# Optimization experiments

Hardware: AMD Instinct MI355X
Metric: run time of the kernel (lower is better)

The kernel has to match this reference:

```python
import jax, jax.numpy as jnp
import numpy as np

N, E, G = 100000, 1600000, 128
IN, HID, HEADS, EDIM, OUT = 16, 32, 4, 8, 4
HC = HEADS * HID


def _p(k, shape):
    return jax.random.normal(k, shape, jnp.float32) * 0.1


def setup_inputs():
    key = jax.random.key(0)
    ks = list(jax.random.split(key, 24))
    nxt = iter(ks)
    d = dict(
        x=jax.random.normal(next(nxt), (N, IN), jnp.float32),
        edge_index=jax.random.randint(next(nxt), (2, E), 0, N),
        edge_attr=jax.random.normal(next(nxt), (E, EDIM), jnp.float32),
        batch=jnp.sort(jax.random.randint(next(nxt), (N,), 0, G)),
    )
    # conv1: in=IN -> heads*hid
    d['wl1'] = _p(next(nxt), (IN, HC));  d['bl1'] = jnp.zeros((HC,), jnp.float32)
    d['wr1'] = _p(next(nxt), (IN, HC));  d['br1'] = jnp.zeros((HC,), jnp.float32)
    d['we1'] = _p(next(nxt), (EDIM, HC)); d['att1'] = _p(next(nxt), (HEADS, HID)); d['bc1'] = jnp.zeros((HC,), jnp.float32)
    # conv2: in=HC -> heads*hid
    d['wl2'] = _p(next(nxt), (HC, HC));  d['bl2'] = jnp.zeros((HC,), jnp.float32)
    d['wr2'] = _p(next(nxt), (HC, HC));  d['br2'] = jnp.zeros((HC,), jnp.float32)
    d['we2'] = _p(next(nxt), (EDIM, HC)); d['att2'] = _p(next(nxt), (HEADS, HID)); d['bc2'] = jnp.zeros((HC,), jnp.float32)
    # conv3: in=HC -> 1*hid (heads=1)
    d['wl3'] = _p(next(nxt), (HC, HID)); d['bl3'] = jnp.zeros((HID,), jnp.float32)
    d['wr3'] = _p(next(nxt), (HC, HID)); d['br3'] = jnp.zeros((HID,), jnp.float32)
    d['we3'] = _p(next(nxt), (EDIM, HID)); d['att3'] = _p(next(nxt), (1, HID)); d['bc3'] = jnp.zeros((HID,), jnp.float32)
    d['w_fc1'] = _p(next(nxt), (HID, 2 * HID)); d['b_fc1'] = jnp.zeros((2 * HID,), jnp.float32)
    d['w_fc2'] = _p(next(nxt), (2 * HID, OUT)); d['b_fc2'] = jnp.zeros((OUT,), jnp.float32)
    return d


def _gatv2(x, src, dst, eattr, wl, bl, wr, br, we, att, bias, n):
    # PyG GATv2Conv: e_ij = a^T . leaky_relu(Wl x_j + Wr x_i + We e_ij)
    H, C = att.shape
    xl = (x @ wl + bl).reshape(-1, H, C)  # source transform [N,H,C]
    xr = (x @ wr + br).reshape(-1, H, C)  # target transform [N,H,C]
    ea = (eattr @ we).reshape(-1, H, C)   # edge transform   [E,H,C]
    e = jax.nn.leaky_relu(xl[src] + xr[dst] + ea, 0.2)  # [E,H,C]
    logit = jnp.einsum('ehc,hc->eh', e, att)            # [E,H]
    m = jax.ops.segment_max(logit, dst, num_segments=n)
    p = jnp.exp(logit - m[dst])
    s = jax.ops.segment_sum(p, dst, num_segments=n)
    alpha = p / (s[dst] + 1e-16)                        # segment softmax per dst
    out = jax.ops.segment_sum(xl[src] * alpha[:, :, None], dst, num_segments=n)
    return out.reshape(n, H * C) + bias


def reference(x, edge_index, edge_attr, batch,
              wl1, bl1, wr1, br1, we1, att1, bc1,
              wl2, bl2, wr2, br2, we2, att2, bc2,
              wl3, bl3, wr3, br3, we3, att3, bc3,
              w_fc1, b_fc1, w_fc2, b_fc2):
    n = x.shape[0]
    src, dst = edge_index[0], edge_index[1]
    # add_self_loops=True with fill_value='mean' (mean of incoming edge_attr per node)
    ones_e = jnp.ones((src.shape[0],), x.dtype)
    cnt = jax.ops.segment_sum(ones_e, dst, num_segments=n)
    loop_attr = jax.ops.segment_sum(edge_attr, dst, num_segments=n) / jnp.maximum(cnt, 1.0)[:, None]
    ar = jnp.arange(n)
    src_a = jnp.concatenate([src, ar])
    dst_a = jnp.concatenate([dst, ar])
    ea = jnp.concatenate([edge_attr, loop_attr], axis=0)

    h = jax.nn.elu(_gatv2(x, src_a, dst_a, ea, wl1, bl1, wr1, br1, we1, att1, bc1, n))
    h = jax.nn.elu(_gatv2(h, src_a, dst_a, ea, wl2, bl2, wr2, br2, we2, att2, bc2, n))
    h = jax.nn.elu(_gatv2(h, src_a, dst_a, ea, wl3, bl3, wr3, br3, we3, att3, bc3, n))

    # global mean pool over graphs
    gs = jax.ops.segment_sum(h, batch, num_segments=G)
    gc = jax.ops.segment_sum(jnp.ones((n,), h.dtype), batch, num_segments=G)
    g = gs / jnp.maximum(gc, 1.0)[:, None]

    g = jax.nn.elu(g @ w_fc1 + b_fc1)
    return g @ w_fc2 + b_fc2
```

## Files before the change

### kernel.cpp

```cpp
#include <hip/hip_runtime.h>
#include <cstdint>
#include <type_traits>

constexpr int GNUM = 128;

typedef _Float16 h2 __attribute__((ext_vector_type(2)));
typedef _Float16 h4 __attribute__((ext_vector_type(4)));
typedef _Float16 h8 __attribute__((ext_vector_type(8)));
typedef float f4 __attribute__((ext_vector_type(4)));


__global__ __launch_bounds__(256) void hist_kernel(const int* __restrict__ dst,
                                                   int* __restrict__ cnt, int E) {
  int i = blockIdx.x * 256 + threadIdx.x;
  if (i < E) atomicAdd(&cnt[dst[i]], 1);
}

__global__ __launch_bounds__(256) void scan_part_kernel(const int* __restrict__ cnt,
                                                        int* __restrict__ bpart, int n) {
  __shared__ int red[256];
  int base = blockIdx.x * 512;
  int t = threadIdx.x;
  int s = 0;
  int i0 = base + t, i1 = base + 256 + t;
  if (i0 < n) s += cnt[i0] + 1;
  if (i1 < n) s += cnt[i1] + 1;
  red[t] = s;
  __syncthreads();
  for (int off = 128; off > 0; off >>= 1) {
    if (t < off) red[t] += red[t + off];
    __syncthreads();
  }
  if (t == 0) bpart[blockIdx.x] = red[0];
}

__global__ __launch_bounds__(1024) void scan_top_kernel(const int* __restrict__ bpart,
                                                        int* __restrict__ boff,
                                                        int* __restrict__ row_ptr,
                                                        int B, int n) {
  __shared__ int buf[1024];
  int t = threadIdx.x;
  buf[t] = (t < B) ? bpart[t] : 0;
  __syncthreads();
  for (int off = 1; off < 1024; off <<= 1) {
    int v = (t >= off) ? buf[t - off] : 0;
    __syncthreads();
    buf[t] += v;
    __syncthreads();
  }
  if (t < B) boff[t] = (t == 0) ? 0 : buf[t - 1];
  if (t == 0) row_ptr[n] = buf[1023];
}

__global__ __launch_bounds__(256) void scan_write_kernel(const int* __restrict__ cnt,
                                                         const int* __restrict__ boff,
                                                         int* __restrict__ row_ptr,
                                                         int* __restrict__ fill, int n) {
  __shared__ int red[256];
  int base = blockIdx.x * 512;
  int t = threadIdx.x;
  int i0 = base + 2 * t, i1 = base + 2 * t + 1;
  int v0 = (i0 < n) ? cnt[i0] + 1 : 0;
  int v1 = (i1 < n) ? cnt[i1] + 1 : 0;
  int val = v0 + v1;
  red[t] = val;
  __syncthreads();
  for (int off = 1; off < 256; off <<= 1) {
    int u = (t >= off) ? red[t - off] : 0;
    __syncthreads();
    red[t] += u;
    __syncthreads();
  }
  int o = boff[blockIdx.x] + red[t] - val;
  if (i0 < n) { row_ptr[i0] = o; fill[i0] = o; }
  if (i1 < n) { row_ptr[i1] = o + v0; fill[i1] = o + v0; }
}

__global__ __launch_bounds__(256) void scatter_kernel(const int* __restrict__ src,
                                                      const int* __restrict__ dst,
                                                      const float* __restrict__ ea,
                                                      int* __restrict__ fill,
                                                      int* __restrict__ csr_src,
                                                      _Float16* __restrict__ ea_csr, int E) {
  int i = blockIdx.x * 256 + threadIdx.x;
  if (i >= E) return;
  int d = dst[i];
  int p = atomicAdd(&fill[d], 1);
  csr_src[p] = src[i];
  float4 e0 = *(const float4*)&ea[(size_t)i * 8];
  float4 e1 = *(const float4*)&ea[(size_t)i * 8 + 4];
  h8 v;
  v[0] = (_Float16)e0.x; v[1] = (_Float16)e0.y; v[2] = (_Float16)e0.z; v[3] = (_Float16)e0.w;
  v[4] = (_Float16)e1.x; v[5] = (_Float16)e1.y; v[6] = (_Float16)e1.z; v[7] = (_Float16)e1.w;
  *(h8*)&ea_csr[(size_t)p * 8] = v;
}

__global__ __launch_bounds__(256) void selfloop_kernel(const int* __restrict__ row_ptr,
                                                       int* __restrict__ csr_src,
                                                       _Float16* __restrict__ ea_csr, int n) {
  int i = blockIdx.x * 256 + threadIdx.x;
  if (i >= n) return;
  int s = row_ptr[i], e = row_ptr[i + 1] - 1;
  float a[8] = {0, 0, 0, 0, 0, 0, 0, 0};
  for (int j = s; j < e; j++) {
    h8 t = *(const h8*)&ea_csr[(size_t)j * 8];
#pragma unroll
    for (int k = 0; k < 8; k++) a[k] += (float)t[k];
  }
  float inv = 1.f / fmaxf((float)(e - s), 1.f);
  h8 o;
#pragma unroll
  for (int k = 0; k < 8; k++) o[k] = (_Float16)(a[k] * inv);
  *(h8*)&ea_csr[(size_t)e * 8] = o;
  csr_src[e] = i;
}

__global__ __launch_bounds__(256) void pack_kernel(const float* __restrict__ w0,
                                                   _Float16* __restrict__ wp0,
                                                   const float* __restrict__ w1,
                                                   _Float16* __restrict__ wp1,
                                                   int K, int NC) {
  const float* w = blockIdx.y ? w1 : w0;
  _Float16* wp = blockIdx.y ? wp1 : wp0;
  int KB = K / 32;
  int total = (NC / 16) * KB * 64;
  int idx = blockIdx.x * 256 + threadIdx.x;
  if (idx >= total) return;
  int lane = idx & 63;
  int blk = idx >> 6;
  int nt = blk / KB, kb = blk % KB;
  int col = nt * 16 + (lane & 15);
  int krow = kb * 32 + (lane >> 4) * 8;
  h8 v;
#pragma unroll
  for (int j = 0; j < 8; j++) v[j] = (_Float16)w[(size_t)(krow + j) * NC + col];
  *(h8*)&wp[(size_t)idx * 8] = v;
}


template <int K, int NCOLS>
__global__ __launch_bounds__(256) void k1_kernel(const float* __restrict__ x,
                                                 const float* __restrict__ w0,
                                                 const float* __restrict__ b0,
                                                 _Float16* __restrict__ out0,
                                                 const float* __restrict__ w1,
                                                 const float* __restrict__ b1,
                                                 _Float16* __restrict__ out1, int n) {
  constexpr int KC = (K < 32) ? K : 32;
  constexpr int CG = NCOLS / 4;
  constexpr int NG = 256 / CG;
  constexpr int MTILE = NG * 8;
  constexpr int XS = KC + 4;
  __shared__ float xs[MTILE * XS];
  __shared__ float ws[KC * NCOLS];

  const float* w = blockIdx.y ? w1 : w0;
  const float* b = blockIdx.y ? b1 : b0;
  _Float16* out = blockIdx.y ? out1 : out0;

  int tid = threadIdx.x;
  int cg = tid % CG, ng = tid / CG;
  int c0 = 4 * cg, n0 = 8 * ng;
  int node0 = blockIdx.x * MTILE;

  float acc[8][4] = {};

  for (int k0 = 0; k0 < K; k0 += KC) {
    for (int idx = tid; idx < MTILE * KC / 4; idx += 256) {
      int nl = idx / (KC / 4), kq = idx % (KC / 4);
      int gn = node0 + nl;
      float4 v = make_float4(0.f, 0.f, 0.f, 0.f);
      if (gn < n) v = *(const float4*)&x[(size_t)gn * K + k0 + 4 * kq];
      *(float4*)&xs[nl * XS + 4 * kq] = v;
    }
    for (int idx = tid; idx < KC * NCOLS / 4; idx += 256) {
      int kr = idx / (NCOLS / 4), cq = idx % (NCOLS / 4);
      *(float4*)&ws[kr * NCOLS + 4 * cq] =
          *(const float4*)&w[(size_t)(k0 + kr) * NCOLS + 4 * cq];
    }
    __syncthreads();
#pragma unroll
    for (int kk = 0; kk < KC; kk += 4) {
      float4 wv0 = *(const float4*)&ws[(kk + 0) * NCOLS + c0];
      float4 wv1 = *(const float4*)&ws[(kk + 1) * NCOLS + c0];
      float4 wv2 = *(const float4*)&ws[(kk + 2) * NCOLS + c0];
      float4 wv3 = *(const float4*)&ws[(kk + 3) * NCOLS + c0];
#pragma unroll
      for (int j = 0; j < 8; j++) {
        float4 xv = *(const float4*)&xs[(n0 + j) * XS + kk];
        acc[j][0] += xv.x * wv0.x + xv.y * wv1.x + xv.z * wv2.x + xv.w * wv3.x;
        acc[j][1] += xv.x * wv0.y + xv.y * wv1.y + xv.z * wv2.y + xv.w * wv3.y;
        acc[j][2] += xv.x * wv0.z + xv.y * wv1.z + xv.z * wv2.z + xv.w * wv3.z;
        acc[j][3] += xv.x * wv0.w + xv.y * wv1.w + xv.z * wv2.w + xv.w * wv3.w;
      }
    }
    __syncthreads();
  }

  float4 bv = *(const float4*)&b[c0];
#pragma unroll
  for (int j = 0; j < 8; j++) {
    int gn = node0 + n0 + j;
    if (gn < n) {
      h4 o;
      o[0] = (_Float16)(acc[j][0] + bv.x);
      o[1] = (_Float16)(acc[j][1] + bv.y);
      o[2] = (_Float16)(acc[j][2] + bv.z);
      o[3] = (_Float16)(acc[j][3] + bv.w);
      *(h4*)&out[(size_t)gn * NCOLS + c0] = o;
    }
  }
}

template <int K, int NCOLS>
__global__ __launch_bounds__(256) void k1m_kernel(const _Float16* __restrict__ x,
                                                  const _Float16* __restrict__ wp0,
                                                  const float* __restrict__ b0,
                                                  _Float16* __restrict__ out0,
                                                  const _Float16* __restrict__ wp1,
                                                  const float* __restrict__ b1,
                                                  _Float16* __restrict__ out1, int n) {
  constexpr int NT = NCOLS / 16, KB = K / 32;
  const _Float16* wp = blockIdx.y ? wp1 : wp0;
  const float* b = blockIdx.y ? b1 : b0;
  _Float16* out = blockIdx.y ? out1 : out0;

  int tid = threadIdx.x;
  int wave = tid >> 6, lane = tid & 63;
  int m = lane & 15, quad = lane >> 4;
  int node0 = blockIdx.x * 64 + wave * 16;

  h8 afrag[KB];
  int anode = node0 + m;
  if (anode < n) {
#pragma unroll
    for (int kb = 0; kb < KB; kb++)
      afrag[kb] = *(const h8*)&x[(size_t)anode * K + kb * 32 + quad * 8];
  } else {
#pragma unroll
    for (int kb = 0; kb < KB; kb++) afrag[kb] = (h8)(_Float16)0.f;
  }

  f4 acc[NT] = {};
#pragma unroll
  for (int nt = 0; nt < NT; nt++) {
#pragma unroll
    for (int kb = 0; kb < KB; kb++) {
      h8 bfrag = *(const h8*)&wp[((size_t)(nt * KB + kb) * 64 + lane) * 8];
      acc[nt] = __builtin_amdgcn_mfma_f32_16x16x32_f16(afrag[kb], bfrag, acc[nt], 0, 0, 0);
    }
  }

#pragma unroll
  for (int nt = 0; nt < NT; nt++) {
#pragma unroll
    for (int r = 0; r < 4; r++) {
      int row = node0 + quad * 4 + r;
      if (row < n) {
        int col = nt * 16 + m;
        out[(size_t)row * NCOLS + col] = (_Float16)(acc[nt][r] + b[col]);
      }
    }
  }
}

template <int H>
__global__ __launch_bounds__(128) void k2_kernel(
    const _Float16* __restrict__ xl, const _Float16* __restrict__ xr,
    const int* __restrict__ row_ptr, const int* __restrict__ csr_src,
    const _Float16* __restrict__ ea_csr, const float* __restrict__ we,
    const float* __restrict__ att, const float* __restrict__ bc,
    _Float16* __restrict__ out, int n) {
  constexpr int HC = H * 32;
  constexpr int NL = HC / 4;
  constexpr int NPB = 128 / NL;

  int tid = threadIdx.x;
  int ln = tid / NL, q = tid % NL;
  int c0 = 4 * q;
  int node = blockIdx.x * NPB + ln;
  if (node >= n) return;

  h2 w2[8][2];
#pragma unroll
  for (int k = 0; k < 8; k++) {
    float4 v = *(const float4*)&we[k * HC + c0];
    w2[k][0] = h2{(_Float16)v.x, (_Float16)v.y};
    w2[k][1] = h2{(_Float16)v.z, (_Float16)v.w};
  }
  const float LOG2E = 1.44269504088896f;
  float4 av = *(const float4*)&att[c0];
  h2 a0 = h2{(_Float16)(av.x * LOG2E), (_Float16)(av.y * LOG2E)};
  h2 a1 = h2{(_Float16)(av.z * LOG2E), (_Float16)(av.w * LOG2E)};
  h4 xrh = *(const h4*)&xr[(size_t)node * HC + c0];
  h2 xr0 = h2{xrh[0], xrh[1]}, xr1 = h2{xrh[2], xrh[3]};
  const h2 p2 = h2{(_Float16)0.2f, (_Float16)0.2f};

  float acc[4] = {0.f, 0.f, 0.f, 0.f};
  float s = 0.f;

  int start = row_ptr[node], end = row_ptr[node + 1];
  for (int j = start; j < end; j++) {
    int src = csr_src[j];
    h8 eh = *(const h8*)&ea_csr[(size_t)j * 8];
    h4 xlh = *(const h4*)&xl[(size_t)src * HC + c0];

    h2 t0 = h2{xlh[0], xlh[1]} + xr0;
    h2 t1 = h2{xlh[2], xlh[3]} + xr1;
#pragma unroll
    for (int k = 0; k < 8; k++) {
      h2 ev = h2{eh[k], eh[k]};
      t0 += ev * w2[k][0];
      t1 += ev * w2[k][1];
    }
    t0 = __builtin_elementwise_max(t0, t0 * p2);
    t1 = __builtin_elementwise_max(t1, t1 * p2);
    h2 pd = t0 * a0 + t1 * a1;
    float part = (float)pd[0] + (float)pd[1];
    part += __shfl_xor(part, 1, 64);
    part += __shfl_xor(part, 2, 64);
    part += __shfl_xor(part, 4, 64);
    float p = __builtin_amdgcn_exp2f(part);
    s += p;
#pragma unroll
    for (int i = 0; i < 4; i++) acc[i] += p * (float)xlh[i];
  }

  float inv = 1.f / (s + 1e-16f);
  h4 o;
#pragma unroll
  for (int i = 0; i < 4; i++) {
    float v = acc[i] * inv + bc[c0 + i];
    o[i] = (_Float16)(v > 0.f ? v : (__expf(v) - 1.f));
  }
  *(h4*)&out[(size_t)node * HC + c0] = o;
}


__global__ __launch_bounds__(256) void gbound_kernel(const int* __restrict__ batch,
                                                     int* __restrict__ gstart, int n) {
  int g = blockIdx.x * 256 + threadIdx.x;
  if (g > GNUM) return;
  int lo = 0, hi = n;
  while (lo < hi) {
    int mid = (lo + hi) >> 1;
    if (batch[mid] < g) lo = mid + 1; else hi = mid;
  }
  gstart[g] = lo;
}

__global__ __launch_bounds__(256) void pool2_kernel(const _Float16* __restrict__ h,
                                                    const int* __restrict__ gstart,
                                                    float* __restrict__ gmean) {
  __shared__ float red[256];
  int g = blockIdx.x;
  int t = threadIdx.x;
  int s = gstart[g], e = gstart[g + 1];
  int c = t & 31, rg = t >> 5;
  float acc = 0.f;
  for (int i = s + rg; i < e; i += 8) acc += (float)h[(size_t)i * 32 + c];
  red[t] = acc;
  __syncthreads();
  if (t < 128) red[t] += red[t + 128];
  __syncthreads();
  if (t < 64) red[t] += red[t + 64];
  __syncthreads();
  if (t < 32) {
    float v = red[t] + red[t + 32];
    gmean[g * 32 + t] = v / fmaxf((float)(e - s), 1.f);
  }
}

__global__ __launch_bounds__(64) void fc_kernel(const float* __restrict__ gmean,
                                                const float* __restrict__ w1,
                                                const float* __restrict__ b1,
                                                const float* __restrict__ w2,
                                                const float* __restrict__ b2,
                                                float* __restrict__ out) {
  __shared__ float g[32];
  __shared__ float a1[64];
  int gi = blockIdx.x;
  int t = threadIdx.x;
  if (t < 32) g[t] = gmean[gi * 32 + t];
  __syncthreads();
  float v = b1[t];
  for (int k = 0; k < 32; k++) v += g[k] * w1[k * 64 + t];
  a1[t] = v > 0.f ? v : (__expf(v) - 1.f);
  __syncthreads();
  if (t < 4) {
    float o = b2[t];
    for (int k = 0; k < 64; k++) o += a1[k] * w2[k * 4 + t];
    out[gi * 4 + t] = o;
  }
}


extern "C" void kernel_launch(void* const* d_in, const int* in_sizes, int n_in,
                              void* d_out, int out_size, void* d_ws, size_t ws_size,
                              hipStream_t stream) {
  const float* x     = (const float*)d_in[0];
  const int*   ei    = (const int*)d_in[1];
  const float* eattr = (const float*)d_in[2];
  const int*   batch = (const int*)d_in[3];
  const float *wl1 = (const float*)d_in[4],  *bl1 = (const float*)d_in[5];
  const float *wr1 = (const float*)d_in[6],  *br1 = (const float*)d_in[7];
  const float *we1 = (const float*)d_in[8],  *at1 = (const float*)d_in[9];
  const float *bc1 = (const float*)d_in[10];
  const float *wl2 = (const float*)d_in[11], *bl2 = (const float*)d_in[12];
  const float *wr2 = (const float*)d_in[13], *br2 = (const float*)d_in[14];
  const float *we2 = (const float*)d_in[15], *at2 = (const float*)d_in[16];
  const float *bc2 = (const float*)d_in[17];
  const float *wl3 = (const float*)d_in[18], *bl3 = (const float*)d_in[19];
  const float *wr3 = (const float*)d_in[20], *br3 = (const float*)d_in[21];
  const float *we3 = (const float*)d_in[22], *at3 = (const float*)d_in[23];
  const float *bc3 = (const float*)d_in[24];
  const float *wf1 = (const float*)d_in[25], *bf1 = (const float*)d_in[26];
  const float *wf2 = (const float*)d_in[27], *bf2 = (const float*)d_in[28];

  int N = in_sizes[0] / 16;
  int E = in_sizes[1] / 2;
  const int* srcp = ei;
  const int* dstp = ei + E;
  int EA = E + N;
  int NB = (N + 511) / 512;

  char* wsb = (char*)d_ws;
  size_t off = 0;
  auto alloc = [&](size_t bytes) -> char* {
    char* p = wsb + off;
    off += (bytes + 255) & ~(size_t)255;
    return p;
  };
  int*       cnt     = (int*)alloc((size_t)N * 4);
  int*       row_ptr = (int*)alloc((size_t)(N + 1) * 4);
  int*       fill    = (int*)alloc((size_t)N * 4);
  int*       bpart   = (int*)alloc((size_t)1024 * 4);
  int*       boff    = (int*)alloc((size_t)1024 * 4);
  int*       csr_src = (int*)alloc((size_t)EA * 4);
  _Float16*  ea_csr  = (_Float16*)alloc((size_t)EA * 8 * 2);
  _Float16*  xl      = (_Float16*)alloc((size_t)N * 128 * 2);
  _Float16*  xr      = (_Float16*)alloc((size_t)N * 128 * 2);
  _Float16*  h16     = (_Float16*)alloc((size_t)N * 128 * 2);
  _Float16*  h3      = (_Float16*)alloc((size_t)N * 32 * 2);
  float*     gmean   = (float*)alloc((size_t)GNUM * 32 * 4);
  int*       gstart  = (int*)alloc((size_t)(GNUM + 1) * 4);
  _Float16*  wp2l    = (_Float16*)alloc((size_t)128 * 128 * 2);
  _Float16*  wp2r    = (_Float16*)alloc((size_t)128 * 128 * 2);
  _Float16*  wp3l    = (_Float16*)alloc((size_t)128 * 32 * 2);
  _Float16*  wp3r    = (_Float16*)alloc((size_t)128 * 32 * 2);

  hipMemsetAsync(cnt, 0, (size_t)N * 4, stream);

  hist_kernel<<<(E + 255) / 256, 256, 0, stream>>>(dstp, cnt, E);
  scan_part_kernel<<<NB, 256, 0, stream>>>(cnt, bpart, N);
  scan_top_kernel<<<1, 1024, 0, stream>>>(bpart, boff, row_ptr, NB, N);
  scan_write_kernel<<<NB, 256, 0, stream>>>(cnt, boff, row_ptr, fill, N);
  scatter_kernel<<<(E + 255) / 256, 256, 0, stream>>>(srcp, dstp, eattr, fill, csr_src, ea_csr, E);
  selfloop_kernel<<<(N + 255) / 256, 256, 0, stream>>>(row_ptr, csr_src, ea_csr, N);
  gbound_kernel<<<1, 256, 0, stream>>>(batch, gstart, N);
  pack_kernel<<<dim3(8, 2), 256, 0, stream>>>(wl2, wp2l, wr2, wp2r, 128, 128);
  pack_kernel<<<dim3(2, 2), 256, 0, stream>>>(wl3, wp3l, wr3, wp3r, 128, 32);

  k1_kernel<16, 128><<<dim3((N + 63) / 64, 2), 256, 0, stream>>>(
      x, wl1, bl1, xl, wr1, br1, xr, N);
  k2_kernel<4><<<(N + 3) / 4, 128, 0, stream>>>(xl, xr, row_ptr, csr_src, ea_csr,
                                                we1, at1, bc1, h16, N);
  k1m_kernel<128, 128><<<dim3((N + 63) / 64, 2), 256, 0, stream>>>(
      h16, wp2l, bl2, xl, wp2r, br2, xr, N);
  k2_kernel<4><<<(N + 3) / 4, 128, 0, stream>>>(xl, xr, row_ptr, csr_src, ea_csr,
                                                we2, at2, bc2, h16, N);
  k1m_kernel<128, 32><<<dim3((N + 63) / 64, 2), 256, 0, stream>>>(
      h16, wp3l, bl3, xl, wp3r, br3, xr, N);
  k2_kernel<1><<<(N + 15) / 16, 128, 0, stream>>>(xl, xr, row_ptr, csr_src, ea_csr,
                                                  we3, at3, bc3, h3, N);

  pool2_kernel<<<GNUM, 256, 0, stream>>>(h3, gstart, gmean);
  fc_kernel<<<GNUM, 64, 0, stream>>>(gmean, wf1, bf1, wf2, bf2, (float*)d_out);
}
```

Measured before the change: 775.8 us.

## Pad CSR rows to multiples of four and prefetch edges in aggregation

Pads each destination's CSR row to a multiple of four, filling the extra slots with -1 sentinels. The aggregation kernel can then process edges four at a time and software-prefetch the next group's indices, edge attributes and source features, hiding gather latency. The first-layer linear transform now uses an MFMA fp16 kernel on x converted to half precision, and the self-loop mean is parallelised across the 8 attribute channels. Costs are extra padded memory, wasted work on padding slots and an additional fp16 rounding of the input features.

```diff
diff --git a/kernel.cpp b/kernel.cpp
--- a/kernel.cpp
+++ b/kernel.cpp
@@ -15,6 +15,8 @@
   int i = blockIdx.x * 256 + threadIdx.x;
   if (i < E) atomicAdd(&cnt[dst[i]], 1);
 }
+
+__device__ __forceinline__ int padlen(int c) { return (c + 4) & ~3; }
 
 __global__ __launch_bounds__(256) void scan_part_kernel(const int* __restrict__ cnt,
                                                         int* __restrict__ bpart, int n) {
@@ -23,8 +25,8 @@
   int t = threadIdx.x;
   int s = 0;
   int i0 = base + t, i1 = base + 256 + t;
-  if (i0 < n) s += cnt[i0] + 1;
-  if (i1 < n) s += cnt[i1] + 1;
+  if (i0 < n) s += padlen(cnt[i0]);
+  if (i1 < n) s += padlen(cnt[i1]);
   red[t] = s;
   __syncthreads();
   for (int off = 128; off > 0; off >>= 1) {
@@ -60,8 +62,8 @@
   int base = blockIdx.x * 512;
   int t = threadIdx.x;
   int i0 = base + 2 * t, i1 = base + 2 * t + 1;
-  int v0 = (i0 < n) ? cnt[i0] + 1 : 0;
-  int v1 = (i1 < n) ? cnt[i1] + 1 : 0;
+  int v0 = (i0 < n) ? padlen(cnt[i0]) : 0;
+  int v1 = (i1 < n) ? padlen(cnt[i1]) : 0;
   int val = v0 + v1;
   red[t] = val;
   __syncthreads();
@@ -96,33 +98,31 @@
 }
 
 __global__ __launch_bounds__(256) void selfloop_kernel(const int* __restrict__ row_ptr,
+                                                       const int* __restrict__ fill,
                                                        int* __restrict__ csr_src,
                                                        _Float16* __restrict__ ea_csr, int n) {
-  int i = blockIdx.x * 256 + threadIdx.x;
+  int idx = blockIdx.x * 256 + threadIdx.x;
+  int i = idx >> 3, c = idx & 7;
   if (i >= n) return;
-  int s = row_ptr[i], e = row_ptr[i + 1] - 1;
-  float a[8] = {0, 0, 0, 0, 0, 0, 0, 0};
-  for (int j = s; j < e; j++) {
-    h8 t = *(const h8*)&ea_csr[(size_t)j * 8];
-#pragma unroll
-    for (int k = 0; k < 8; k++) a[k] += (float)t[k];
-  }
-  float inv = 1.f / fmaxf((float)(e - s), 1.f);
-  h8 o;
-#pragma unroll
-  for (int k = 0; k < 8; k++) o[k] = (_Float16)(a[k] * inv);
-  *(h8*)&ea_csr[(size_t)e * 8] = o;
-  csr_src[e] = i;
+  int s = row_ptr[i], sf = fill[i], e = row_ptr[i + 1];
+  float a = 0.f;
+  for (int j = s; j < sf; j++) a += (float)ea_csr[(size_t)j * 8 + c];
+  float inv = 1.f / fmaxf((float)(sf - s), 1.f);
+  ea_csr[(size_t)sf * 8 + c] = (_Float16)(a * inv);
+  if (c == 0) {
+    csr_src[sf] = i;
+    for (int p = sf + 1; p < e; p++) csr_src[p] = -1;
+  }
 }
 
 __global__ __launch_bounds__(256) void pack_kernel(const float* __restrict__ w0,
                                                    _Float16* __restrict__ wp0,
                                                    const float* __restrict__ w1,
                                                    _Float16* __restrict__ wp1,
-                                                   int K, int NC) {
+                                                   int Kreal, int Kpad, int NC) {
   const float* w = blockIdx.y ? w1 : w0;
   _Float16* wp = blockIdx.y ? wp1 : wp0;
-  int KB = K / 32;
+  int KB = Kpad / 32;
   int total = (NC / 16) * KB * 64;
   int idx = blockIdx.x * 256 + threadIdx.x;
   if (idx >= total) return;
@@ -133,84 +133,21 @@
   int krow = kb * 32 + (lane >> 4) * 8;
   h8 v;
 #pragma unroll
-  for (int j = 0; j < 8; j++) v[j] = (_Float16)w[(size_t)(krow + j) * NC + col];
+  for (int j = 0; j < 8; j++)
+    v[j] = (krow + j < Kreal) ? (_Float16)w[(size_t)(krow + j) * NC + col] : (_Float16)0.f;
   *(h8*)&wp[(size_t)idx * 8] = v;
 }
 
-
-template <int K, int NCOLS>
-__global__ __launch_bounds__(256) void k1_kernel(const float* __restrict__ x,
-                                                 const float* __restrict__ w0,
-                                                 const float* __restrict__ b0,
-                                                 _Float16* __restrict__ out0,
-                                                 const float* __restrict__ w1,
-                                                 const float* __restrict__ b1,
-                                                 _Float16* __restrict__ out1, int n) {
-  constexpr int KC = (K < 32) ? K : 32;
-  constexpr int CG = NCOLS / 4;
-  constexpr int NG = 256 / CG;
-  constexpr int MTILE = NG * 8;
-  constexpr int XS = KC + 4;
-  __shared__ float xs[MTILE * XS];
-  __shared__ float ws[KC * NCOLS];
-
-  const float* w = blockIdx.y ? w1 : w0;
-  const float* b = blockIdx.y ? b1 : b0;
-  _Float16* out = blockIdx.y ? out1 : out0;
-
-  int tid = threadIdx.x;
-  int cg = tid % CG, ng = tid / CG;
-  int c0 = 4 * cg, n0 = 8 * ng;
-  int node0 = blockIdx.x * MTILE;
-
-  float acc[8][4] = {};
-
-  for (int k0 = 0; k0 < K; k0 += KC) {
-    for (int idx = tid; idx < MTILE * KC / 4; idx += 256) {
-      int nl = idx / (KC / 4), kq = idx % (KC / 4);
-      int gn = node0 + nl;
-      float4 v = make_float4(0.f, 0.f, 0.f, 0.f);
-      if (gn < n) v = *(const float4*)&x[(size_t)gn * K + k0 + 4 * kq];
-      *(float4*)&xs[nl * XS + 4 * kq] = v;
-    }
-    for (int idx = tid; idx < KC * NCOLS / 4; idx += 256) {
-      int kr = idx / (NCOLS / 4), cq = idx % (NCOLS / 4);
-      *(float4*)&ws[kr * NCOLS + 4 * cq] =
-          *(const float4*)&w[(size_t)(k0 + kr) * NCOLS + 4 * cq];
-    }
-    __syncthreads();
-#pragma unroll
-    for (int kk = 0; kk < KC; kk += 4) {
-      float4 wv0 = *(const float4*)&ws[(kk + 0) * NCOLS + c0];
-      float4 wv1 = *(const float4*)&ws[(kk + 1) * NCOLS + c0];
-      float4 wv2 = *(const float4*)&ws[(kk + 2) * NCOLS + c0];
-      float4 wv3 = *(const float4*)&ws[(kk + 3) * NCOLS + c0];
-#pragma unroll
-      for (int j = 0; j < 8; j++) {
-        float4 xv = *(const float4*)&xs[(n0 + j) * XS + kk];
-        acc[j][0] += xv.x * wv0.x + xv.y * wv1.x + xv.z * wv2.x + xv.w * wv3.x;
-        acc[j][1] += xv.x * wv0.y + xv.y * wv1.y + xv.z * wv2.y + xv.w * wv3.y;
-        acc[j][2] += xv.x * wv0.z + xv.y * wv1.z + xv.z * wv2.z + xv.w * wv3.z;
-        acc[j][3] += xv.x * wv0.w + xv.y * wv1.w + xv.z * wv2.w + xv.w * wv3.w;
-      }
-    }
-    __syncthreads();
-  }
-
-  float4 bv = *(const float4*)&b[c0];
-#pragma unroll
-  for (int j = 0; j < 8; j++) {
-    int gn = node0 + n0 + j;
-    if (gn < n) {
-      h4 o;
-      o[0] = (_Float16)(acc[j][0] + bv.x);
-      o[1] = (_Float16)(acc[j][1] + bv.y);
-      o[2] = (_Float16)(acc[j][2] + bv.z);
-      o[3] = (_Float16)(acc[j][3] + bv.w);
-      *(h4*)&out[(size_t)gn * NCOLS + c0] = o;
-    }
-  }
-}
+__global__ __launch_bounds__(256) void cvt16_kernel(const float* __restrict__ x,
+                                                    _Float16* __restrict__ x16, int total4) {
+  int i = blockIdx.x * 256 + threadIdx.x;
+  if (i >= total4) return;
+  float4 v = ((const float4*)x)[i];
+  h4 o;
+  o[0] = (_Float16)v.x; o[1] = (_Float16)v.y; o[2] = (_Float16)v.z; o[3] = (_Float16)v.w;
+  ((h4*)x16)[i] = o;
+}
+
 
 template <int K, int NCOLS>
 __global__ __launch_bounds__(256) void k1m_kernel(const _Float16* __restrict__ x,
@@ -264,6 +201,51 @@
   }
 }
 
+template <int NCOLS>
+__global__ __launch_bounds__(256) void k1m16_kernel(const _Float16* __restrict__ x16,
+                                                    const _Float16* __restrict__ wp0,
+                                                    const float* __restrict__ b0,
+                                                    _Float16* __restrict__ out0,
+                                                    const _Float16* __restrict__ wp1,
+                                                    const float* __restrict__ b1,
+                                                    _Float16* __restrict__ out1, int n) {
+  constexpr int NT = NCOLS / 16;
+  const _Float16* wp = blockIdx.y ? wp1 : wp0;
+  const float* b = blockIdx.y ? b1 : b0;
+  _Float16* out = blockIdx.y ? out1 : out0;
+
+  int tid = threadIdx.x;
+  int wave = tid >> 6, lane = tid & 63;
+  int m = lane & 15, quad = lane >> 4;
+  int node0 = blockIdx.x * 64 + wave * 16;
+
+  int anode = node0 + m;
+  h8 afrag;
+  if (anode < n && quad < 2)
+    afrag = *(const h8*)&x16[(size_t)anode * 16 + quad * 8];
+  else
+    afrag = (h8)(_Float16)0.f;
+
+  f4 acc[NT] = {};
+#pragma unroll
+  for (int nt = 0; nt < NT; nt++) {
+    h8 bfrag = *(const h8*)&wp[((size_t)nt * 64 + lane) * 8];
+    acc[nt] = __builtin_amdgcn_mfma_f32_16x16x32_f16(afrag, bfrag, acc[nt], 0, 0, 0);
+  }
+
+#pragma unroll
+  for (int nt = 0; nt < NT; nt++) {
+#pragma unroll
+    for (int r = 0; r < 4; r++) {
+      int row = node0 + quad * 4 + r;
+      if (row < n) {
+        int col = nt * 16 + m;
+        out[(size_t)row * NCOLS + col] = (_Float16)(acc[nt][r] + b[col]);
+      }
+    }
+  }
+}
+
 template <int H>
 __global__ __launch_bounds__(128) void k2_kernel(
     const _Float16* __restrict__ xl, const _Float16* __restrict__ xr,
@@ -300,30 +282,68 @@
   float s = 0.f;
 
   int start = row_ptr[node], end = row_ptr[node + 1];
-  for (int j = start; j < end; j++) {
-    int src = csr_src[j];
-    h8 eh = *(const h8*)&ea_csr[(size_t)j * 8];
-    h4 xlh = *(const h4*)&xl[(size_t)src * HC + c0];
-
-    h2 t0 = h2{xlh[0], xlh[1]} + xr0;
-    h2 t1 = h2{xlh[2], xlh[3]} + xr1;
-#pragma unroll
-    for (int k = 0; k < 8; k++) {
-      h2 ev = h2{eh[k], eh[k]};
-      t0 += ev * w2[k][0];
-      t1 += ev * w2[k][1];
-    }
-    t0 = __builtin_elementwise_max(t0, t0 * p2);
-    t1 = __builtin_elementwise_max(t1, t1 * p2);
-    h2 pd = t0 * a0 + t1 * a1;
-    float part = (float)pd[0] + (float)pd[1];
-    part += __shfl_xor(part, 1, 64);
-    part += __shfl_xor(part, 2, 64);
-    part += __shfl_xor(part, 4, 64);
-    float p = __builtin_amdgcn_exp2f(part);
-    s += p;
-#pragma unroll
-    for (int i = 0; i < 4; i++) acc[i] += p * (float)xlh[i];
+
+  int cs[4]; h8 ce[4]; h4 cx[4];
+#pragma unroll
+  for (int e = 0; e < 4; e++) {
+    cs[e] = csr_src[start + e];
+    ce[e] = *(const h8*)&ea_csr[(size_t)(start + e) * 8];
+  }
+#pragma unroll
+  for (int e = 0; e < 4; e++) {
+    int sx = cs[e] < 0 ? 0 : cs[e];
+    cx[e] = *(const h4*)&xl[(size_t)sx * HC + c0];
+  }
+
+  for (int j = start; j < end; j += 4) {
+    int jn = (j + 4 < end) ? j + 4 : start;
+    int ns[4]; h8 ne[4]; h4 nx[4];
+#pragma unroll
+    for (int e = 0; e < 4; e++) {
+      ns[e] = csr_src[jn + e];
+      ne[e] = *(const h8*)&ea_csr[(size_t)(jn + e) * 8];
+    }
+
+    float part[4];
+#pragma unroll
+    for (int e = 0; e < 4; e++) {
+      h2 t0 = h2{cx[e][0], cx[e][1]} + xr0;
+      h2 t1 = h2{cx[e][2], cx[e][3]} + xr1;
+#pragma unroll
+      for (int k = 0; k < 8; k++) {
+        h2 ev = h2{ce[e][k], ce[e][k]};
+        t0 += ev * w2[k][0];
+        t1 += ev * w2[k][1];
+      }
+      t0 = __builtin_elementwise_max(t0, t0 * p2);
+      t1 = __builtin_elementwise_max(t1, t1 * p2);
+      h2 pd = t0 * a0 + t1 * a1;
+      part[e] = (float)pd[0] + (float)pd[1];
+    }
+
+#pragma unroll
+    for (int e = 0; e < 4; e++) {
+      int sx = ns[e] < 0 ? 0 : ns[e];
+      nx[e] = *(const h4*)&xl[(size_t)sx * HC + c0];
+    }
+
+#pragma unroll
+    for (int e = 0; e < 4; e++) part[e] += __shfl_xor(part[e], 1, 64);
+#pragma unroll
+    for (int e = 0; e < 4; e++) part[e] += __shfl_xor(part[e], 2, 64);
+#pragma unroll
+    for (int e = 0; e < 4; e++) part[e] += __shfl_xor(part[e], 4, 64);
+
+#pragma unroll
+    for (int e = 0; e < 4; e++) {
+      float p = (cs[e] >= 0) ? __builtin_amdgcn_exp2f(part[e]) : 0.f;
+      s += p;
+#pragma unroll
+      for (int i = 0; i < 4; i++) acc[i] += p * (float)cx[e][i];
+    }
+
+#pragma unroll
+    for (int e = 0; e < 4; e++) { cs[e] = ns[e]; ce[e] = ne[e]; cx[e] = nx[e]; }
   }
 
   float inv = 1.f / (s + 1e-16f);
@@ -421,7 +441,7 @@
   int E = in_sizes[1] / 2;
   const int* srcp = ei;
   const int* dstp = ei + E;
-  int EA = E + N;
+  int EApad = E + 4 * N;
   int NB = (N + 511) / 512;
 
   char* wsb = (char*)d_ws;
@@ -436,14 +456,17 @@
   int*       fill    = (int*)alloc((size_t)N * 4);
   int*       bpart   = (int*)alloc((size_t)1024 * 4);
   int*       boff    = (int*)alloc((size_t)1024 * 4);
-  int*       csr_src = (int*)alloc((size_t)EA * 4);
-  _Float16*  ea_csr  = (_Float16*)alloc((size_t)EA * 8 * 2);
+  int*       csr_src = (int*)alloc((size_t)EApad * 4);
+  _Float16*  ea_csr  = (_Float16*)alloc((size_t)EApad * 8 * 2);
   _Float16*  xl      = (_Float16*)alloc((size_t)N * 128 * 2);
   _Float16*  xr      = (_Float16*)alloc((size_t)N * 128 * 2);
   _Float16*  h16     = (_Float16*)alloc((size_t)N * 128 * 2);
   _Float16*  h3      = (_Float16*)alloc((size_t)N * 32 * 2);
+  _Float16*  x16     = (_Float16*)alloc((size_t)N * 16 * 2);
   float*     gmean   = (float*)alloc((size_t)GNUM * 32 * 4);
   int*       gstart  = (int*)alloc((size_t)(GNUM + 1) * 4);
+  _Float16*  wp1l    = (_Float16*)alloc((size_t)32 * 128 * 2);
+  _Float16*  wp1r    = (_Float16*)alloc((size_t)32 * 128 * 2);
   _Float16*  wp2l    = (_Float16*)alloc((size_t)128 * 128 * 2);
   _Float16*  wp2r    = (_Float16*)alloc((size_t)128 * 128 * 2);
   _Float16*  wp3l    = (_Float16*)alloc((size_t)128 * 32 * 2);
@@ -456,13 +479,15 @@
   scan_top_kernel<<<1, 1024, 0, stream>>>(bpart, boff, row_ptr, NB, N);
   scan_write_kernel<<<NB, 256, 0, stream>>>(cnt, boff, row_ptr, fill, N);
   scatter_kernel<<<(E + 255) / 256, 256, 0, stream>>>(srcp, dstp, eattr, fill, csr_src, ea_csr, E);
-  selfloop_kernel<<<(N + 255) / 256, 256, 0, stream>>>(row_ptr, csr_src, ea_csr, N);
+  selfloop_kernel<<<(N * 8 + 255) / 256, 256, 0, stream>>>(row_ptr, fill, csr_src, ea_csr, N);
   gbound_kernel<<<1, 256, 0, stream>>>(batch, gstart, N);
-  pack_kernel<<<dim3(8, 2), 256, 0, stream>>>(wl2, wp2l, wr2, wp2r, 128, 128);
-  pack_kernel<<<dim3(2, 2), 256, 0, stream>>>(wl3, wp3l, wr3, wp3r, 128, 32);
-
-  k1_kernel<16, 128><<<dim3((N + 63) / 64, 2), 256, 0, stream>>>(
-      x, wl1, bl1, xl, wr1, br1, xr, N);
+  cvt16_kernel<<<(N * 4 + 255) / 256, 256, 0, stream>>>(x, x16, N * 4);
+  pack_kernel<<<dim3(2, 2), 256, 0, stream>>>(wl1, wp1l, wr1, wp1r, 16, 32, 128);
+  pack_kernel<<<dim3(8, 2), 256, 0, stream>>>(wl2, wp2l, wr2, wp2r, 128, 128, 128);
+  pack_kernel<<<dim3(2, 2), 256, 0, stream>>>(wl3, wp3l, wr3, wp3r, 128, 128, 32);
+
+  k1m16_kernel<128><<<dim3((N + 63) / 64, 2), 256, 0, stream>>>(
+      x16, wp1l, bl1, xl, wp1r, br1, xr, N);
   k2_kernel<4><<<(N + 3) / 4, 128, 0, stream>>>(xl, xr, row_ptr, csr_src, ea_csr,
                                                 we1, at1, bc1, h16, N);
   k1m_kernel<128, 128><<<dim3((N + 63) / 64, 2), 256, 0, stream>>>(
```

Measured after the change: 752.8 us. 3.0% less time.
